# Kernel optimization log

Hardware: AMD Instinct MI355X
Metric: run time of the kernel (lower is better)

Reference implementation:

```python
import jax, jax.numpy as jnp
import numpy as np

N = 12                      # total wires
LAYERS = 2
INIT_W = [0, 1, 2]
PK_W = [3, 4, 5, 6, 7]
PD_W = [8, 9, 10, 11]
KEYS = ['init_euler', 'pk_coup', 'pd_coup', 'pk_local', 'pd_local']
SHAPES = [(LAYERS, 3, 3), (LAYERS, 3, 5), (LAYERS, 3, 4), (LAYERS, 5), (LAYERS, 4)]
# Assumed physiological bounds (DEFAULT_PK_BOUNDS / DEFAULT_PD_BOUNDS not in snippet)
PK_BOUNDS = np.array([[0.1, 5.0], [1.0, 20.0], [10.0, 100.0], [0.05, 2.0], [0.1, 10.0]], dtype=np.float32)
PD_BOUNDS = np.array([[0.01, 1.0], [0.1, 5.0], [1.0, 50.0], [0.05, 2.0]], dtype=np.float32)
X_GATE = jnp.array([[0, 1], [1, 0]], dtype=jnp.complex64)


def ry(t):
    c, s = jnp.cos(t / 2), jnp.sin(t / 2)
    return jnp.stack([jnp.stack([c, -s], -1), jnp.stack([s, c], -1)], -2).astype(jnp.complex64)


def rx(t):
    c, s = jnp.cos(t / 2), jnp.sin(t / 2)
    return jnp.stack([jnp.stack([c + 0j, -1j * s], -1), jnp.stack([-1j * s, c + 0j], -1)], -2).astype(jnp.complex64)


def rz(t):
    em, ep = jnp.exp(-1j * t / 2), jnp.exp(1j * t / 2)
    z = jnp.zeros_like(em)
    return jnp.stack([jnp.stack([em, z], -1), jnp.stack([z, ep], -1)], -2).astype(jnp.complex64)


def apply_1q(state, gate, w):
    # state: (B, 2^N); gate: (2,2) shared or (B,2,2) per-sample
    B = state.shape[0]
    s = state.reshape(B, 2 ** w, 2, 2 ** (N - 1 - w))
    if gate.ndim == 3:
        s = jnp.einsum('bij,bxjy->bxiy', gate, s)
    else:
        s = jnp.einsum('ij,bxjy->bxiy', gate, s)
    return s.reshape(B, -1)


def apply_ctrl(state, gate, c, t):
    # controlled-gate: apply 2x2 `gate` on target wire t where control wire c == 1
    B = state.shape[0]
    a, b = (c, t) if c < t else (t, c)
    s = state.reshape(B, 2 ** a, 2, 2 ** (b - a - 1), 2, 2 ** (N - 1 - b))
    if c < t:
        sub = jnp.einsum('ij,bamjc->bamic', gate, s[:, :, 1])
        s = s.at[:, :, 1].set(sub)
    else:
        sub = jnp.einsum('ij,bajmc->baimc', gate, s[:, :, :, :, 1])
        s = s.at[:, :, :, :, 1].set(sub)
    return s.reshape(B, -1)


def expz(state, w):
    B = state.shape[0]
    p = (state.real ** 2 + state.imag ** 2).reshape(B, 2 ** w, 2, 2 ** (N - 1 - w))
    p = p.sum(axis=(1, 3))  # (B, 2)
    return p[:, 0] - p[:, 1]


def _unpack(theta):
    w, off = {}, 0
    for name, shape in zip(KEYS, SHAPES):
        size = int(np.prod(shape))
        w[name] = theta[off:off + size].reshape(shape)
        off += size
    return w


def _forward(covariates, dose_intensities, theta):
    inputs = jnp.concatenate([covariates, dose_intensities[:, None]], axis=1).astype(jnp.float32)  # (B, 3)
    B = inputs.shape[0]
    state = jnp.zeros((B, 2 ** N), jnp.complex64).at[:, 0].set(1.0)
    # input encoding: per-sample RY angles on init wires
    for i, w in enumerate(INIT_W):
        state = apply_1q(state, ry(inputs[:, i]), w)
    wd = _unpack(theta)
    for l in range(LAYERS):
        for q in range(3):
            e = wd['init_euler'][l, q]
            state = apply_1q(state, rx(e[0]), INIT_W[q])
            state = apply_1q(state, ry(e[1]), INIT_W[q])
            state = apply_1q(state, rz(e[2]), INIT_W[q])
        state = apply_ctrl(state, X_GATE, INIT_W[0], INIT_W[1])
        state = apply_ctrl(state, X_GATE, INIT_W[1], INIT_W[2])
        state = apply_ctrl(state, X_GATE, INIT_W[2], INIT_W[0])
        for i in range(3):
            for j in range(5):
                state = apply_ctrl(state, ry(wd['pk_coup'][l, i, j]), INIT_W[i], PK_W[j])
        for j in range(5):
            state = apply_1q(state, ry(wd['pk_local'][l, j]), PK_W[j])
        for i in range(3):
            for k in range(4):
                state = apply_ctrl(state, ry(wd['pd_coup'][l, i, k]), INIT_W[i], PD_W[k])
        for k in range(4):
            state = apply_1q(state, ry(wd['pd_local'][l, k]), PD_W[k])
    raw = jnp.stack([expz(state, w) for w in PK_W + PD_W], axis=1)  # (B, 9)
    s = 0.5 * (raw + 1.0)
    pk = PK_BOUNDS[:, 0] + s[:, :5] * (PK_BOUNDS[:, 1] - PK_BOUNDS[:, 0])
    pd = PD_BOUNDS[:, 0] + s[:, 5:] * (PD_BOUNDS[:, 1] - PD_BOUNDS[:, 0])
    return pk, pd


def setup_inputs() -> dict:
    key = jax.random.key(0)
    k1, k2, k3, k4 = jax.random.split(key, 4)
    B = 512
    return {
        'subject_ids': jax.random.randint(k1, (B,), 0, B),
        'covariates': jax.random.normal(k2, (B, 2), dtype=jnp.float32),
        'dose_intensities': jax.random.uniform(k3, (B,), dtype=jnp.float32),
        'theta': jax.random.normal(k4, (90,), dtype=jnp.float32) * 0.1,
    }


def reference(subject_ids, covariates, dose_intensities, theta):
    return _forward(covariates, dose_intensities, theta)
```

## Files before the change

kernel.cpp:

```cpp
#include <hip/hip_runtime.h>
#include <math.h>

#define NT 576

__global__ __launch_bounds__(NT)
void qpkpd_kernel(const float* __restrict__ cov,
                  const float* __restrict__ dose,
                  const float* __restrict__ theta,
                  float* __restrict__ out, int B)
{
    __shared__ float  sA0[72];
    __shared__ float2 sCS1[72];
    __shared__ float  sV1r[64], sV1i[64];
    __shared__ float2 sV0T[64];
    __shared__ float  sCD[576];
    __shared__ float2 sP2[512];
    __shared__ float2 sG2[576];
    __shared__ float2 sMT[576];
    __shared__ float  sS[576];
    __shared__ float  sTf[252];

    const int t = threadIdx.x;

    float q0[3], q1[3], q2[3];
    int bS = 0;
    if (t >= 512) {
        bS = blockIdx.x * 64 + (t - 512);
        float2 xy = ((const float2*)cov)[bS];
        float xd = dose[bS];
        float h0 = 0.5f*xy.x, h1 = 0.5f*xy.y, h2 = 0.5f*xd;
        float s0=__sinf(h0), c0=__cosf(h0);
        float s1=__sinf(h1), c1=__cosf(h1);
        float s2=__sinf(h2), c2=__cosf(h2);
        q0[0]=c0*c0; q0[1]=c0*s0; q0[2]=s0*s0;
        q1[0]=c1*c1; q1[1]=c1*s1; q1[2]=s1*s1;
        q2[0]=c2*c2; q2[1]=c2*s2; q2[2]=s2*s2;
    }

    if (t < 128) {
        int l = t >> 6, rc = t & 63;
        int r = rc >> 3, c = rc & 7;
        float tr = 1.f, ti = 0.f;
        #pragma unroll
        for (int q = 0; q < 3; ++q) {
            float h0 = 0.5f*theta[l*9 + q*3 + 0];
            float h1 = 0.5f*theta[l*9 + q*3 + 1];
            float h2 = 0.5f*theta[l*9 + q*3 + 2];
            float s0=__sinf(h0), c0=__cosf(h0);
            float s1=__sinf(h1), c1=__cosf(h1);
            float s2=__sinf(h2), c2=__cosf(h2);
            int a = (r >> (2-q)) & 1, bb = (c >> (2-q)) & 1;
            float rab  = (a==bb) ? c1 : (a ? s1 : -s1);
            float ra1b = (a!=bb) ? c1 : (a ? s1 : -s1);
            float mr = rab*c0, mi = -ra1b*s0;
            float sa = a ? -1.f : 1.f;
            float er = mr*c2 + sa*mi*s2;
            float ei = mi*c2 - sa*mr*s2;
            float nr = tr*er - ti*ei;
            ti = tr*ei + ti*er;
            tr = nr;
        }
        int rb0=(r>>2)&1, rb1=(r>>1)&1, rb2=r&1;
        int nb1 = rb1 ^ rb0, nb2 = rb2 ^ nb1, nb0 = rb0 ^ nb2;
        int pr = (nb0<<2)|(nb1<<1)|nb2;
        if (l == 0) sV0T[c*8 + pr] = make_float2(tr, ti);
        else { sV1r[pr*8 + c] = tr; sV1i[pr*8 + c] = ti; }
    } else if (t < 200) {
        int idx = t - 128;
        int w = idx >> 3, c = idx & 7;
        float b0 = (float)((c>>2)&1), b1 = (float)((c>>1)&1), b2 = (float)(c&1);
        float a0, a1;
        if (w < 5) {
            a0 = theta[72 + w] + b0*theta[18 + w] + b1*theta[23 + w] + b2*theta[28 + w];
            a1 = theta[77 + w] + b0*theta[33 + w] + b1*theta[38 + w] + b2*theta[43 + w];
        } else {
            int k = w - 5;
            a0 = theta[82 + k] + b0*theta[48 + k] + b1*theta[52 + k] + b2*theta[56 + k];
            a1 = theta[86 + k] + b0*theta[60 + k] + b1*theta[64 + k] + b2*theta[68 + k];
        }
        sA0[idx] = a0;
        sCS1[idx] = make_float2(__cosf(a1), __sinf(a1));
    }
    __syncthreads();

    {
        int v = t >> 6, p = t & 63;
        sCD[t] = __cosf(0.5f*(sA0[v*8 + (p>>3)] - sA0[v*8 + (p&7)]));
    }
    if (t < 512) {
        int cp = t >> 6, p = t & 63;
        int c1 = p >> 3, c2 = p & 7;
        float r1 = sV1r[cp*8+c1], i1 = sV1i[cp*8+c1];
        float r2 = sV1r[cp*8+c2], i2 = sV1i[cp*8+c2];
        sP2[t] = make_float2(r1*r2 + i1*i2, i1*r2 - r1*i2);
    }
    __syncthreads();

    {
        int w = t >> 6, p = t & 63;
        int c1 = p >> 3, c2 = p & 7;
        float sh = 0.5f*(sA0[w*8+c1] + sA0[w*8+c2]);
        float ssh = __sinf(sh), csh = __cosf(sh);
        float C = 1.f;
        #pragma unroll
        for (int v = 0; v < 9; ++v) {
            float f = sCD[v*64 + p];
            C *= (v == w) ? 1.f : f;
        }
        float P = C*csh, Q = C*ssh;
        const float4* cs4 = (const float4*)(&sCS1[w*8]);
        float4 csa = cs4[0], csb = cs4[1], csc = cs4[2], csd = cs4[3];
        float cw[8] = {csa.x,csa.z,csb.x,csb.z,csc.x,csc.z,csd.x,csd.z};
        float sw[8] = {csa.y,csa.w,csb.y,csb.w,csc.y,csc.w,csd.y,csd.w};
        float Kr=0.f, Ki=0.f, Lr=0.f, Li=0.f;
        #pragma unroll
        for (int cp = 0; cp < 8; ++cp) {
            float2 pp = sP2[cp*64 + p];
            Kr += cw[cp]*pp.x; Ki += cw[cp]*pp.y;
            Lr += sw[cp]*pp.x; Li += sw[cp]*pp.y;
        }
        sG2[t] = make_float2(P*Kr - Q*Lr, P*Ki - Q*Li);
    }
    __syncthreads();

    {
        int w = t >> 6, rc = t & 63, k1 = rc >> 3, c = rc & 7;
        const float4* gp = (const float4*)(&sG2[w*64 + k1*8]);
        const float4* vp = (const float4*)(&sV0T[c*8]);
        float mr = 0.f, mi = 0.f;
        #pragma unroll
        for (int i = 0; i < 4; ++i) {
            float4 g = gp[i];
            float4 v = vp[i];
            mr += g.x*v.x + g.y*v.y + g.z*v.z + g.w*v.w;
            mi += g.y*v.x - g.x*v.y + g.w*v.z - g.z*v.w;
        }
        sMT[w*64 + c*8 + k1] = make_float2(mr, mi);
    }
    __syncthreads();

    {
        int w = t >> 6, rc = t & 63, r = rc >> 3, c = rc & 7;
        const float4* vp = (const float4*)(&sV0T[r*8]);
        const float4* mp = (const float4*)(&sMT[w*64 + c*8]);
        float s = 0.f;
        #pragma unroll
        for (int i = 0; i < 4; ++i) {
            float4 v = vp[i], m = mp[i];
            s += v.x*m.x - v.y*m.y + v.z*m.z - v.w*m.w;
        }
        sS[w*64 + r*8 + c] = s;
    }
    __syncthreads();

    if (t < 243) {
        const float sc[9] = {2.45f, 9.5f, 45.0f, 0.975f, 4.95f,
                             0.495f, 2.45f, 24.5f, 0.975f};
        int w = t / 27, rem = t % 27;
        int j = rem / 9, k = (rem / 3) % 3, l = rem % 3;
        float s = 0.f;
        #pragma unroll
        for (int aj = 0; aj < 2; ++aj) {
            bool vj = (j == 1) || (aj == 0);
            int a0b = (j == 2) || (j == 1 && aj == 1);
            int b0b = (j == 2) || (j == 1 && aj == 0);
            #pragma unroll
            for (int ak = 0; ak < 2; ++ak) {
                bool vk = (k == 1) || (ak == 0);
                int a1b = (k == 2) || (k == 1 && ak == 1);
                int b1b = (k == 2) || (k == 1 && ak == 0);
                #pragma unroll
                for (int al = 0; al < 2; ++al) {
                    bool vl = (l == 1) || (al == 0);
                    int a2b = (l == 2) || (l == 1 && al == 1);
                    int b2b = (l == 2) || (l == 1 && al == 0);
                    if (vj && vk && vl) {
                        int r = a0b*4 + a1b*2 + a2b;
                        int c = b0b*4 + b1b*2 + b2b;
                        s += sS[w*64 + r*8 + c];
                    }
                }
            }
        }
        sTf[w*28 + rem] = s * sc[w];
    }
    if (t >= 256 && t < 265) sTf[(t-256)*28 + 27] = 0.f;
    __syncthreads();

    if (t >= 512 && bS < B) {
        float4 m4[7];
        float* m = (float*)m4;
        #pragma unroll
        for (int j = 0; j < 3; ++j) {
            #pragma unroll
            for (int k = 0; k < 3; ++k) {
                float r = q0[j]*q1[k];
                #pragma unroll
                for (int l = 0; l < 3; ++l)
                    m[j*9 + k*3 + l] = r*q2[l];
            }
        }
        m[27] = 0.f;
        const float off[9] = {2.55f, 10.5f, 55.0f, 1.025f, 5.05f,
                              0.505f, 2.55f, 25.5f, 1.025f};
        #pragma unroll
        for (int w = 0; w < 9; ++w) {
            float g = off[w];
            const float4* tp = (const float4*)(&sTf[w*28]);
            #pragma unroll
            for (int i = 0; i < 7; ++i) {
                float4 tt = tp[i];
                float4 mm = m4[i];
                g += tt.x*mm.x + tt.y*mm.y + tt.z*mm.z + tt.w*mm.w;
            }
            if (w < 5) out[bS*5 + w] = g;
            else       out[B*5 + bS*4 + (w-5)] = g;
        }
    }
}

extern "C" void kernel_launch(void* const* d_in, const int* in_sizes, int n_in,
                              void* d_out, int out_size, void* d_ws, size_t ws_size,
                              hipStream_t stream)
{
    const float* cov   = (const float*)d_in[1];
    const float* dose  = (const float*)d_in[2];
    const float* theta = (const float*)d_in[3];
    float* out = (float*)d_out;
    const int B = in_sizes[2];

    qpkpd_kernel<<<8, NT, 0, stream>>>(cov, dose, theta, out, B);
}
```

Before: 10.43 us.

## Fuse per-wire stages into wave-local pipeline and process whole batch per block

Each wavefront now owns one wire and runs the G2, MT, S and Tf stages back to back through LDS, with no block barriers between them. This removes four __syncthreads. The cos-difference table and the V1 outer-product precompute are dropped; the kernel now reads V1 and the A0 angles directly and calls __cosf inline. Batch handling moves so each block's first 512 threads each handle one sample, which cuts the grid from 8 blocks to ceil(B/512). This avoids recomputing the shared theta-dependent matrices in every block, at the cost of more per-thread transcendental work. Correctness depends on wavefront-local ordering of LDS accesses within the same wave.

Result: slower. 10.64 us (+2.0%).

```diff
diff --git a/kernel.cpp b/kernel.cpp
--- a/kernel.cpp
+++ b/kernel.cpp
@@ -9,32 +9,26 @@
                   const float* __restrict__ theta,
                   float* __restrict__ out, int B)
 {
-    __shared__ float  sA0[72];
+    __shared__ float  sA0T[96];
     __shared__ float2 sCS1[72];
-    __shared__ float  sV1r[64], sV1i[64];
     __shared__ float2 sV0T[64];
-    __shared__ float  sCD[576];
-    __shared__ float2 sP2[512];
+    __shared__ float2 sV1T[64];
     __shared__ float2 sG2[576];
     __shared__ float2 sMT[576];
     __shared__ float  sS[576];
     __shared__ float  sTf[252];
 
-    const int t = threadIdx.x;
-
-    float q0[3], q1[3], q2[3];
-    int bS = 0;
-    if (t >= 512) {
-        bS = blockIdx.x * 64 + (t - 512);
-        float2 xy = ((const float2*)cov)[bS];
-        float xd = dose[bS];
-        float h0 = 0.5f*xy.x, h1 = 0.5f*xy.y, h2 = 0.5f*xd;
-        float s0=__sinf(h0), c0=__cosf(h0);
-        float s1=__sinf(h1), c1=__cosf(h1);
-        float s2=__sinf(h2), c2=__cosf(h2);
-        q0[0]=c0*c0; q0[1]=c0*s0; q0[2]=s0*s0;
-        q1[0]=c1*c1; q1[1]=c1*s1; q1[2]=s1*s1;
-        q2[0]=c2*c2; q2[1]=c2*s2; q2[2]=s2*s2;
+    const int t  = threadIdx.x;
+    const int wv = t >> 6;
+    const int p  = t & 63;
+
+    float2 xy = make_float2(0.f, 0.f);
+    float  xd = 0.f;
+    int b = blockIdx.x * 512 + t;
+    bool ev = (t < 512) && (b < B);
+    if (ev) {
+        xy = ((const float2*)cov)[b];
+        xd = dose[b];
     }
 
     if (t < 128) {
@@ -64,7 +58,7 @@
         int nb1 = rb1 ^ rb0, nb2 = rb2 ^ nb1, nb0 = rb0 ^ nb2;
         int pr = (nb0<<2)|(nb1<<1)|nb2;
         if (l == 0) sV0T[c*8 + pr] = make_float2(tr, ti);
-        else { sV1r[pr*8 + c] = tr; sV1i[pr*8 + c] = ti; }
+        else        sV1T[c*8 + pr] = make_float2(tr, ti);
     } else if (t < 200) {
         int idx = t - 128;
         int w = idx >> 3, c = idx & 7;
@@ -78,129 +72,129 @@
             a0 = theta[82 + k] + b0*theta[48 + k] + b1*theta[52 + k] + b2*theta[56 + k];
             a1 = theta[86 + k] + b0*theta[60 + k] + b1*theta[64 + k] + b2*theta[68 + k];
         }
-        sA0[idx] = a0;
+        sA0T[c*12 + w] = a0;
         sCS1[idx] = make_float2(__cosf(a1), __sinf(a1));
     }
     __syncthreads();
 
     {
-        int v = t >> 6, p = t & 63;
-        sCD[t] = __cosf(0.5f*(sA0[v*8 + (p>>3)] - sA0[v*8 + (p&7)]));
-    }
-    if (t < 512) {
-        int cp = t >> 6, p = t & 63;
-        int c1 = p >> 3, c2 = p & 7;
-        float r1 = sV1r[cp*8+c1], i1 = sV1i[cp*8+c1];
-        float r2 = sV1r[cp*8+c2], i2 = sV1i[cp*8+c2];
-        sP2[t] = make_float2(r1*r2 + i1*i2, i1*r2 - r1*i2);
-    }
-    __syncthreads();
-
-    {
-        int w = t >> 6, p = t & 63;
-        int c1 = p >> 3, c2 = p & 7;
-        float sh = 0.5f*(sA0[w*8+c1] + sA0[w*8+c2]);
-        float ssh = __sinf(sh), csh = __cosf(sh);
-        float C = 1.f;
+        const int w = wv;
+        const int r = p >> 3, c = p & 7;
+
+        const float4* a4r = (const float4*)(&sA0T[r*12]);
+        const float4* a4c = (const float4*)(&sA0T[c*12]);
+        float4 A, Bv;
+        float ar_[9], ac_[9];
+        A = a4r[0]; ar_[0]=A.x; ar_[1]=A.y; ar_[2]=A.z; ar_[3]=A.w;
+        A = a4r[1]; ar_[4]=A.x; ar_[5]=A.y; ar_[6]=A.z; ar_[7]=A.w;
+        ar_[8] = sA0T[r*12 + 8];
+        Bv = a4c[0]; ac_[0]=Bv.x; ac_[1]=Bv.y; ac_[2]=Bv.z; ac_[3]=Bv.w;
+        Bv = a4c[1]; ac_[4]=Bv.x; ac_[5]=Bv.y; ac_[6]=Bv.z; ac_[7]=Bv.w;
+        ac_[8] = sA0T[c*12 + 8];
+
+        float C = 1.f, sh = 0.f;
         #pragma unroll
         for (int v = 0; v < 9; ++v) {
-            float f = sCD[v*64 + p];
-            C *= (v == w) ? 1.f : f;
-        }
-        float P = C*csh, Q = C*ssh;
+            if (v == w) sh = 0.5f*(ar_[v] + ac_[v]);
+            else        C *= __cosf(0.5f*(ar_[v] - ac_[v]));
+        }
+        float P = C*__cosf(sh), Q = C*__sinf(sh);
+
+        const float4* v1r = (const float4*)(&sV1T[r*8]);
+        const float4* v1c = (const float4*)(&sV1T[c*8]);
         const float4* cs4 = (const float4*)(&sCS1[w*8]);
-        float4 csa = cs4[0], csb = cs4[1], csc = cs4[2], csd = cs4[3];
-        float cw[8] = {csa.x,csa.z,csb.x,csb.z,csc.x,csc.z,csd.x,csd.z};
-        float sw[8] = {csa.y,csa.w,csb.y,csb.w,csc.y,csc.w,csd.y,csd.w};
         float Kr=0.f, Ki=0.f, Lr=0.f, Li=0.f;
         #pragma unroll
-        for (int cp = 0; cp < 8; ++cp) {
-            float2 pp = sP2[cp*64 + p];
-            Kr += cw[cp]*pp.x; Ki += cw[cp]*pp.y;
-            Lr += sw[cp]*pp.x; Li += sw[cp]*pp.y;
-        }
-        sG2[t] = make_float2(P*Kr - Q*Lr, P*Ki - Q*Li);
-    }
-    __syncthreads();
-
-    {
-        int w = t >> 6, rc = t & 63, k1 = rc >> 3, c = rc & 7;
-        const float4* gp = (const float4*)(&sG2[w*64 + k1*8]);
-        const float4* vp = (const float4*)(&sV0T[c*8]);
+        for (int i = 0; i < 4; ++i) {
+            float4 a = v1r[i];
+            float4 bq = v1c[i];
+            float4 cs = cs4[i];
+            float pr0 = a.x*bq.x + a.y*bq.y, pi0 = a.y*bq.x - a.x*bq.y;
+            float pr1 = a.z*bq.z + a.w*bq.w, pi1 = a.w*bq.z - a.z*bq.w;
+            Kr += cs.x*pr0 + cs.z*pr1;  Ki += cs.x*pi0 + cs.z*pi1;
+            Lr += cs.y*pr0 + cs.w*pr1;  Li += cs.y*pi0 + cs.w*pi1;
+        }
+        sG2[w*64 + p] = make_float2(P*Kr - Q*Lr, P*Ki - Q*Li);
+
+        const float4* gp = (const float4*)(&sG2[w*64 + r*8]);
+        const float4* vc = (const float4*)(&sV0T[c*8]);
         float mr = 0.f, mi = 0.f;
         #pragma unroll
         for (int i = 0; i < 4; ++i) {
             float4 g = gp[i];
-            float4 v = vp[i];
+            float4 v = vc[i];
             mr += g.x*v.x + g.y*v.y + g.z*v.z + g.w*v.w;
             mi += g.y*v.x - g.x*v.y + g.w*v.z - g.z*v.w;
         }
-        sMT[w*64 + c*8 + k1] = make_float2(mr, mi);
-    }
-    __syncthreads();
-
-    {
-        int w = t >> 6, rc = t & 63, r = rc >> 3, c = rc & 7;
-        const float4* vp = (const float4*)(&sV0T[r*8]);
-        const float4* mp = (const float4*)(&sMT[w*64 + c*8]);
+        sMT[w*64 + c*8 + r] = make_float2(mr, mi);
+
+        const float4* vr4 = (const float4*)(&sV0T[r*8]);
+        const float4* mp  = (const float4*)(&sMT[w*64 + c*8]);
         float s = 0.f;
         #pragma unroll
         for (int i = 0; i < 4; ++i) {
-            float4 v = vp[i], m = mp[i];
+            float4 v = vr4[i], m = mp[i];
             s += v.x*m.x - v.y*m.y + v.z*m.z - v.w*m.w;
         }
-        sS[w*64 + r*8 + c] = s;
-    }
-    __syncthreads();
-
-    if (t < 243) {
-        const float sc[9] = {2.45f, 9.5f, 45.0f, 0.975f, 4.95f,
-                             0.495f, 2.45f, 24.5f, 0.975f};
-        int w = t / 27, rem = t % 27;
-        int j = rem / 9, k = (rem / 3) % 3, l = rem % 3;
-        float s = 0.f;
-        #pragma unroll
-        for (int aj = 0; aj < 2; ++aj) {
-            bool vj = (j == 1) || (aj == 0);
-            int a0b = (j == 2) || (j == 1 && aj == 1);
-            int b0b = (j == 2) || (j == 1 && aj == 0);
+        sS[w*64 + p] = s;
+
+        if (p < 27) {
+            const float sc[9] = {2.45f, 9.5f, 45.0f, 0.975f, 4.95f,
+                                 0.495f, 2.45f, 24.5f, 0.975f};
+            int j = p / 9, k = (p / 3) % 3, l = p % 3;
+            float acc = 0.f;
             #pragma unroll
-            for (int ak = 0; ak < 2; ++ak) {
-                bool vk = (k == 1) || (ak == 0);
-                int a1b = (k == 2) || (k == 1 && ak == 1);
-                int b1b = (k == 2) || (k == 1 && ak == 0);
+            for (int aj = 0; aj < 2; ++aj) {
+                bool vj = (j == 1) || (aj == 0);
+                int a0b = (j == 2) || (j == 1 && aj == 1);
+                int b0b = (j == 2) || (j == 1 && aj == 0);
                 #pragma unroll
-                for (int al = 0; al < 2; ++al) {
-                    bool vl = (l == 1) || (al == 0);
-                    int a2b = (l == 2) || (l == 1 && al == 1);
-                    int b2b = (l == 2) || (l == 1 && al == 0);
-                    if (vj && vk && vl) {
-                        int r = a0b*4 + a1b*2 + a2b;
-                        int c = b0b*4 + b1b*2 + b2b;
-                        s += sS[w*64 + r*8 + c];
+                for (int ak = 0; ak < 2; ++ak) {
+                    bool vk = (k == 1) || (ak == 0);
+                    int a1b = (k == 2) || (k == 1 && ak == 1);
+                    int b1b = (k == 2) || (k == 1 && ak == 0);
+                    #pragma unroll
+                    for (int al = 0; al < 2; ++al) {
+                        bool vl = (l == 1) || (al == 0);
+                        int a2b = (l == 2) || (l == 1 && al == 1);
+                        int b2b = (l == 2) || (l == 1 && al == 0);
+                        if (vj && vk && vl) {
+                            int rr = a0b*4 + a1b*2 + a2b;
+                            int cc = b0b*4 + b1b*2 + b2b;
+                            acc += sS[w*64 + rr*8 + cc];
+                        }
                     }
                 }
             }
-        }
-        sTf[w*28 + rem] = s * sc[w];
-    }
-    if (t >= 256 && t < 265) sTf[(t-256)*28 + 27] = 0.f;
+            sTf[w*28 + p] = acc * sc[w];
+        }
+        if (p == 27) sTf[w*28 + 27] = 0.f;
+    }
     __syncthreads();
 
-    if (t >= 512 && bS < B) {
+    if (ev) {
+        float h0 = 0.5f*xy.x, h1 = 0.5f*xy.y, h2 = 0.5f*xd;
+        float s0=__sinf(h0), c0=__cosf(h0);
+        float s1=__sinf(h1), c1=__cosf(h1);
+        float s2=__sinf(h2), c2=__cosf(h2);
+        float q0[3] = {c0*c0, c0*s0, s0*s0};
+        float q1[3] = {c1*c1, c1*s1, s1*s1};
+        float q2[3] = {c2*c2, c2*s2, s2*s2};
+
         float4 m4[7];
         float* m = (float*)m4;
         #pragma unroll
         for (int j = 0; j < 3; ++j) {
             #pragma unroll
             for (int k = 0; k < 3; ++k) {
-                float r = q0[j]*q1[k];
+                float rr = q0[j]*q1[k];
                 #pragma unroll
                 for (int l = 0; l < 3; ++l)
-                    m[j*9 + k*3 + l] = r*q2[l];
+                    m[j*9 + k*3 + l] = rr*q2[l];
             }
         }
         m[27] = 0.f;
+
         const float off[9] = {2.55f, 10.5f, 55.0f, 1.025f, 5.05f,
                               0.505f, 2.55f, 25.5f, 1.025f};
         #pragma unroll
@@ -213,8 +207,8 @@
                 float4 mm = m4[i];
                 g += tt.x*mm.x + tt.y*mm.y + tt.z*mm.z + tt.w*mm.w;
             }
-            if (w < 5) out[bS*5 + w] = g;
-            else       out[B*5 + bS*4 + (w-5)] = g;
+            if (w < 5) out[b*5 + w] = g;
+            else       out[B*5 + b*4 + (w-5)] = g;
         }
     }
 }
@@ -229,5 +223,6 @@
     float* out = (float*)d_out;
     const int B = in_sizes[2];
 
-    qpkpd_kernel<<<8, NT, 0, stream>>>(cov, dose, theta, out, B);
+    int grid = (B + 511) / 512;
+    qpkpd_kernel<<<grid, NT, 0, stream>>>(cov, dose, theta, out, B);
 }
```
